# Optimization experiments

Hardware: AMD Instinct MI355X
Metric: run time of the kernel (lower is better)

The kernel has to match this reference:

```python
import jax, jax.numpy as jnp
import numpy as np

IN_BIT = 8      # in_bit_width
W_BIT = 2       # weight_bit_width (also output act quantizer bit width)
BN_EPS = 1e-4


def _ste(x, q):
    # straight-through estimator: forward = q, backward = identity w.r.t. x
    return x + jax.lax.stop_gradient(q - x)


def act_quant(x, bit):
    # CommonActQuant: signed int quant, narrow_range=False, power-of-two scale
    # range [-1, 1 - 2^{-(bit-1)}] -> scale = 2^{-(bit-1)}
    s = 2.0 ** (1 - bit)
    n_min = -(2.0 ** (bit - 1))
    n_max = 2.0 ** (bit - 1) - 1.0
    q = jnp.clip(jnp.round(x / s), n_min, n_max) * s
    return _ste(x, q)


def weight_quant(w, bit):
    # CommonWeightQuant: narrow-range signed int quant, unit scaling const
    # scale = 1 / (2^{bit-1} - 1); for bit=2 levels are {-1, 0, 1}
    n = 2.0 ** (bit - 1) - 1.0
    s = 1.0 / n
    q = jnp.clip(jnp.round(w / s), -n, n) * s
    return _ste(w, q)


def setup_inputs() -> dict:
    key = jax.random.key(0)
    k1, k2, k3, k4 = jax.random.split(key, 4)
    B, C, H, W = 32, 256, 32, 32
    x = jax.random.normal(k1, (B, C, H, W), dtype=jnp.float32) * 0.5
    weight = jax.random.normal(k2, (C, C, 3, 3), dtype=jnp.float32) * 0.5
    gamma = jnp.ones((C,), dtype=jnp.float32)
    beta = jnp.zeros((C,), dtype=jnp.float32)
    running_mean = jax.random.normal(k3, (C,), dtype=jnp.float32) * 0.1
    running_var = jax.random.uniform(k4, (C,), dtype=jnp.float32, minval=0.5, maxval=1.5)
    return {"x": x, "weight": weight, "gamma": gamma, "beta": beta,
            "running_mean": running_mean, "running_var": running_var}


def reference(x, weight, gamma, beta, running_mean, running_var):
    # 1) input QuantIdentity (8-bit, [-1, 1-2^-7], power-of-two scale 2^-7)
    xq = act_quant(x, IN_BIT)
    # 2) QuantConv2d 3x3 stride 1 pad 1, no bias, 2-bit weights
    wq = weight_quant(weight, W_BIT)
    y = jax.lax.conv_general_dilated(
        xq, wq, window_strides=(1, 1), padding=((1, 1), (1, 1)),
        dimension_numbers=("NCHW", "OIHW", "NCHW"))
    # 3) BatchNorm2d (inference, eps=1e-4)
    inv = gamma / jnp.sqrt(running_var + BN_EPS)
    y = y * inv[None, :, None, None] + (beta - running_mean * inv)[None, :, None, None]
    # 4) output QuantIdentity at weight_bit_width bits
    return act_quant(y, W_BIT)
```

## Files before the change

### kernel.cpp

```cpp
#include <hip/hip_runtime.h>
#include <hip/hip_bf16.h>
#include <stdint.h>


typedef int i32x4 __attribute__((ext_vector_type(4)));
typedef float f32x4 __attribute__((ext_vector_type(4)));

__device__ __forceinline__ void gload_lds16(const void* g, const void* lds_byte_ptr) {
    __builtin_amdgcn_global_load_lds(
        (const __attribute__((address_space(1))) unsigned int*)(uintptr_t)g,
        (__attribute__((address_space(3))) unsigned int*)(uintptr_t)lds_byte_ptr,
        16, 0, 0);
}

__global__ __launch_bounds__(256) void quant_w_kernel(const float* __restrict__ w,
                                                      signed char* __restrict__ wq) {
    __shared__ signed char tile[2304];
    const int co = blockIdx.x;
    const int t = threadIdx.x;
#pragma unroll
    for (int p = 0; p < 9; ++p) {
        const int idx = p * 256 + t;
        const float v = w[co * 2304 + idx];
        const int ci = idx / 9;
        const int khkw = idx - 9 * ci;
        const float q = fminf(fmaxf(rintf(v), -1.f), 1.f);
        tile[khkw * 256 + ci] = (signed char)(int)q;
    }
    __syncthreads();
    if (t < 144) {
        *(uint4*)(wq + (size_t)co * 2304 + t * 16) = *(const uint4*)(tile + t * 16);
    }
}

__global__ __launch_bounds__(256) void quant_x_kernel(const float* __restrict__ x,
                                                      signed char* __restrict__ xpad) {
    __shared__ signed char tile[32 * 272];
    const int t = threadIdx.x;
    const int b = blockIdx.x / 34;
    const int hp = blockIdx.x % 34;
    signed char* rowbase = xpad + (size_t)((b * 34 + hp) * 34) * 256;
    const uint4 z = {0u, 0u, 0u, 0u};
    if (hp == 0 || hp == 33) {
        for (int i = t; i < 544; i += 256) *(uint4*)(rowbase + i * 16) = z;
        return;
    }
    const int h = hp - 1;
    const int w = t & 31;
    const int cg = (t >> 5) * 4;
#pragma unroll
    for (int p = 0; p < 8; ++p) {
        const int ci = p * 32 + cg;
        unsigned packed = 0;
#pragma unroll
        for (int k = 0; k < 4; ++k) {
            const float v = x[(((size_t)(b * 256 + ci + k)) * 32 + h) * 32 + w];
            float q = fminf(fmaxf(rintf(__fmul_rn(v, 128.f)), -128.f), 127.f);
            packed |= ((unsigned)(unsigned char)(signed char)(int)q) << (8 * k);
        }
        *(unsigned*)(tile + w * 272 + ci) = packed;
    }
    __syncthreads();
#pragma unroll
    for (int q = 0; q < 2; ++q) {
        const int wp = q * 16 + (t >> 4);
        const int ci16 = (t & 15) * 16;
        uint4 v = *(const uint4*)(tile + wp * 272 + ci16);
        *(uint4*)(rowbase + (size_t)(wp + 1) * 256 + ci16) = v;
    }
    if (t < 32) {
        const int wp = (t >> 4) * 33;
        *(uint4*)(rowbase + (size_t)wp * 256 + (t & 15) * 16) = z;
    }
}

__global__ __launch_bounds__(512) void conv_gemm_kernel(
    const signed char* __restrict__ xpad, const signed char* __restrict__ wq,
    const float* __restrict__ gamma, const float* __restrict__ beta,
    const float* __restrict__ mean, const float* __restrict__ var,
    float* __restrict__ out)
{
    __shared__ signed char As[128 * 64];
    __shared__ signed char Bs[128 * 64];

    const int tid = threadIdx.x;
    const int wv = tid >> 6;
    const int lane = tid & 63;
    const int quad = lane >> 4;
    const int l16 = lane & 15;

    const int m0 = (blockIdx.x >> 1) * 128;
    const int n0 = (blockIdx.x & 1) * 128;
    const int wave_m = wv & 1;
    const int wave_n = wv >> 1;

    i32x4 acc[4][2];
#pragma unroll
    for (int i = 0; i < 4; i++)
#pragma unroll
        for (int j = 0; j < 2; j++) acc[i][j] = (i32x4){0, 0, 0, 0};

    const int srow = tid >> 2;
    const int scic = (tid & 3) * 16;
    const unsigned ldsOff = (unsigned)(wv * 1024);
    const int sb = (m0 + srow) >> 10;
    const int sh = ((m0 + srow) >> 5) & 31;
    const int sw = (m0 + srow) & 31;

    for (int kt = 0; kt < 36; ++kt) {
        const int khkw = kt >> 2;
        const int kh = khkw / 3;
        const int kw = khkw - 3 * kh;
        const int ci0 = (kt & 3) * 64;
        const signed char* ga =
            xpad + (size_t)(((sb * 34 + sh + kh) * 34) + (sw + kw)) * 256 + ci0 + scic;
        gload_lds16(ga, As + ldsOff);
        const signed char* gb = wq + (size_t)(n0 + srow) * 2304 + kt * 64 + scic;
        gload_lds16(gb, Bs + ldsOff);
        __syncthreads();

        i32x4 af[4], bfr[2];
#pragma unroll
        for (int i = 0; i < 4; i++) {
            const int row = wave_m * 64 + i * 16 + l16;
            af[i] = *(const i32x4*)(As + row * 64 + quad * 16);
        }
#pragma unroll
        for (int j = 0; j < 2; j++) {
            const int row = wave_n * 32 + j * 16 + l16;
            bfr[j] = *(const i32x4*)(Bs + row * 64 + quad * 16);
        }
#pragma unroll
        for (int i = 0; i < 4; i++)
#pragma unroll
            for (int j = 0; j < 2; j++)
                acc[i][j] = __builtin_amdgcn_mfma_i32_16x16x64_i8(af[i], bfr[j], acc[i][j], 0, 0, 0);
        __syncthreads();
    }

#pragma unroll
    for (int j = 0; j < 2; j++) {
        const int co = n0 + wave_n * 32 + j * 16 + l16;
        const float iv = __fdiv_rn(gamma[co], __fsqrt_rn(__fadd_rn(var[co], 1e-4f)));
        const float bias = __fsub_rn(beta[co], __fmul_rn(mean[co], iv));
#pragma unroll
        for (int i = 0; i < 4; i++) {
            const int m_base = m0 + wave_m * 64 + i * 16 + quad * 4;
            const int b = m_base >> 10;
            const int h = (m_base >> 5) & 31;
            const int w = m_base & 31;
            f32x4 v;
#pragma unroll
            for (int r = 0; r < 4; r++) {
                const float y = __fmul_rn((float)acc[i][j][r], 0.0078125f);
                const float t = __fadd_rn(__fmul_rn(y, iv), bias);
                float z = rintf(__fmul_rn(t, 2.f));
                z = fminf(fmaxf(z, -2.f), 1.f);
                v[r] = __fmul_rn(z, 0.5f);
            }
            *(f32x4*)(&out[(((size_t)(b * 256 + co)) * 32 + h) * 32 + w]) = v;
        }
    }
}

extern "C" void kernel_launch(void* const* d_in, const int* in_sizes, int n_in,
                              void* d_out, int out_size, void* d_ws, size_t ws_size,
                              hipStream_t stream) {
    const float* x      = (const float*)d_in[0];
    const float* weight = (const float*)d_in[1];
    const float* gamma  = (const float*)d_in[2];
    const float* beta   = (const float*)d_in[3];
    const float* rmean  = (const float*)d_in[4];
    const float* rvar   = (const float*)d_in[5];
    float* out = (float*)d_out;

    signed char* wq   = (signed char*)d_ws;
    signed char* xpad = (signed char*)d_ws + (1 << 20);

    quant_w_kernel<<<256, 256, 0, stream>>>(weight, wq);
    quant_x_kernel<<<1088, 256, 0, stream>>>(x, xpad);
    conv_gemm_kernel<<<512, 512, 0, stream>>>(xpad, wq, gamma, beta, rmean, rvar, out);
}
```

Measured before the change: 123.5 us.

## Stage input halo tile once in LDS and stream pre-swizzled weights from global

The conv GEMM now loads each block's 6x34x256 padded input halo into LDS once, with an XOR swizzle, instead of re-staging an A tile on each of 36 k-steps. This reuses the data across the nine filter taps and removes the per-iteration __syncthreads. The weight quant kernel writes weights in an MFMA-fragment-friendly layout so each wave reads B fragments directly from global memory with double-buffered registers. The trade-off is about 52KB of LDS per block, which can limit occupancy, and more global traffic for the B operand.

```diff
diff --git a/kernel.cpp b/kernel.cpp
--- a/kernel.cpp
+++ b/kernel.cpp
@@ -6,10 +6,10 @@
 typedef int i32x4 __attribute__((ext_vector_type(4)));
 typedef float f32x4 __attribute__((ext_vector_type(4)));
 
-__device__ __forceinline__ void gload_lds16(const void* g, const void* lds_byte_ptr) {
+__device__ __forceinline__ void gload_lds16(const void* g, const void* lds) {
     __builtin_amdgcn_global_load_lds(
         (const __attribute__((address_space(1))) unsigned int*)(uintptr_t)g,
-        (__attribute__((address_space(3))) unsigned int*)(uintptr_t)lds_byte_ptr,
+        (__attribute__((address_space(3))) unsigned int*)(uintptr_t)lds,
         16, 0, 0);
 }
 
@@ -29,7 +29,9 @@
     }
     __syncthreads();
     if (t < 144) {
-        *(uint4*)(wq + (size_t)co * 2304 + t * 16) = *(const uint4*)(tile + t * 16);
+        const int kt = t >> 2, kq = t & 3;
+        const uint4 v = *(const uint4*)(tile + t * 16);
+        *(uint4*)(wq + ((size_t)((co >> 4) * 36 + kt) << 10) + kq * 256 + (co & 15) * 16) = v;
     }
 }
 
@@ -74,25 +76,43 @@
     }
 }
 
-__global__ __launch_bounds__(512) void conv_gemm_kernel(
-    const signed char* __restrict__ xpad, const signed char* __restrict__ wq,
+__global__ __launch_bounds__(512, 4) void conv_gemm_kernel(
+    const signed char* __restrict__ xpad, const signed char* __restrict__ wqm,
     const float* __restrict__ gamma, const float* __restrict__ beta,
     const float* __restrict__ mean, const float* __restrict__ var,
     float* __restrict__ out)
 {
-    __shared__ signed char As[128 * 64];
-    __shared__ signed char Bs[128 * 64];
+    __shared__ signed char As[6 * 34 * 256];
 
     const int tid = threadIdx.x;
     const int wv = tid >> 6;
     const int lane = tid & 63;
-    const int quad = lane >> 4;
     const int l16 = lane & 15;
+    const int l4 = lane >> 4;
 
-    const int m0 = (blockIdx.x >> 1) * 128;
+    const int mt = blockIdx.x >> 1;
     const int n0 = (blockIdx.x & 1) * 128;
+    const int b = mt >> 3;
+    const int h0 = (mt & 7) * 4;
     const int wave_m = wv & 1;
     const int wave_n = wv >> 1;
+
+    const signed char* xbase = xpad + (size_t)(b * 34 + h0) * 34 * 256;
+    for (int i = wv; i < 51; i += 8) {
+        const int d = i * 64 + lane;
+        const int r = d >> 4;
+        const int c = d & 15;
+        gload_lds16(xbase + r * 256 + ((c ^ (r & 15)) << 4), As + i * 1024);
+    }
+    __syncthreads();
+
+    int r0[4];
+#pragma unroll
+    for (int i = 0; i < 4; ++i)
+        r0[i] = (wave_m * 2 + (i >> 1)) * 34 + (i & 1) * 16 + l16;
+
+    const signed char* bp0 = wqm + (((size_t)((n0 >> 4) + wave_n * 2 + 0) * 36) << 10) + lane * 16;
+    const signed char* bp1 = wqm + (((size_t)((n0 >> 4) + wave_n * 2 + 1) * 36) << 10) + lane * 16;
 
     i32x4 acc[4][2];
 #pragma unroll
@@ -100,55 +120,45 @@
 #pragma unroll
         for (int j = 0; j < 2; j++) acc[i][j] = (i32x4){0, 0, 0, 0};
 
-    const int srow = tid >> 2;
-    const int scic = (tid & 3) * 16;
-    const unsigned ldsOff = (unsigned)(wv * 1024);
-    const int sb = (m0 + srow) >> 10;
-    const int sh = ((m0 + srow) >> 5) & 31;
-    const int sw = (m0 + srow) & 31;
+    i32x4 aA[4], bA[2], aB[4], bB[2];
 
-    for (int kt = 0; kt < 36; ++kt) {
-        const int khkw = kt >> 2;
-        const int kh = khkw / 3;
-        const int kw = khkw - 3 * kh;
-        const int ci0 = (kt & 3) * 64;
-        const signed char* ga =
-            xpad + (size_t)(((sb * 34 + sh + kh) * 34) + (sw + kw)) * 256 + ci0 + scic;
-        gload_lds16(ga, As + ldsOff);
-        const signed char* gb = wq + (size_t)(n0 + srow) * 2304 + kt * 64 + scic;
-        gload_lds16(gb, Bs + ldsOff);
-        __syncthreads();
+#define LOAD_B(kt, dst) { dst[0] = *(const i32x4*)(bp0 + (kt) * 1024); \
+                          dst[1] = *(const i32x4*)(bp1 + (kt) * 1024); }
+#define LOAD_A(kt, dst) { const int khkw = (kt) >> 2; \
+                          const int kh = khkw / 3; \
+                          const int kw = khkw - 3 * kh; \
+                          const int roff = kh * 34 + kw; \
+                          const int cb = ((kt) & 3) * 4 + l4; \
+                          _Pragma("unroll") \
+                          for (int i = 0; i < 4; ++i) { \
+                              const int r = r0[i] + roff; \
+                              dst[i] = *(const i32x4*)(As + r * 256 + ((cb ^ (r & 15)) << 4)); \
+                          } }
+#define MFMA(af, bf) { _Pragma("unroll") \
+                       for (int i = 0; i < 4; ++i) \
+                           _Pragma("unroll") \
+                           for (int j = 0; j < 2; ++j) \
+                               acc[i][j] = __builtin_amdgcn_mfma_i32_16x16x64_i8(af[i], bf[j], acc[i][j], 0, 0, 0); }
 
-        i32x4 af[4], bfr[2];
-#pragma unroll
-        for (int i = 0; i < 4; i++) {
-            const int row = wave_m * 64 + i * 16 + l16;
-            af[i] = *(const i32x4*)(As + row * 64 + quad * 16);
-        }
-#pragma unroll
-        for (int j = 0; j < 2; j++) {
-            const int row = wave_n * 32 + j * 16 + l16;
-            bfr[j] = *(const i32x4*)(Bs + row * 64 + quad * 16);
-        }
-#pragma unroll
-        for (int i = 0; i < 4; i++)
-#pragma unroll
-            for (int j = 0; j < 2; j++)
-                acc[i][j] = __builtin_amdgcn_mfma_i32_16x16x64_i8(af[i], bfr[j], acc[i][j], 0, 0, 0);
-        __syncthreads();
+    LOAD_B(0, bA)
+    LOAD_A(0, aA)
+    for (int kt = 0; kt < 36; kt += 2) {
+        LOAD_B(kt + 1, bB)
+        LOAD_A(kt + 1, aB)
+        MFMA(aA, bA)
+        if (kt + 2 < 36) { LOAD_B(kt + 2, bA) LOAD_A(kt + 2, aA) }
+        MFMA(aB, bB)
     }
 
 #pragma unroll
-    for (int j = 0; j < 2; j++) {
+    for (int j = 0; j < 2; ++j) {
         const int co = n0 + wave_n * 32 + j * 16 + l16;
         const float iv = __fdiv_rn(gamma[co], __fsqrt_rn(__fadd_rn(var[co], 1e-4f)));
         const float bias = __fsub_rn(beta[co], __fmul_rn(mean[co], iv));
 #pragma unroll
-        for (int i = 0; i < 4; i++) {
-            const int m_base = m0 + wave_m * 64 + i * 16 + quad * 4;
-            const int b = m_base >> 10;
-            const int h = (m_base >> 5) & 31;
-            const int w = m_base & 31;
+        for (int i = 0; i < 4; ++i) {
+            const int h = h0 + wave_m * 2 + (i >> 1);
+            const int w = (i & 1) * 16 + l4 * 4;
             f32x4 v;
 #pragma unroll
             for (int r = 0; r < 4; r++) {
@@ -161,6 +171,9 @@
             *(f32x4*)(&out[(((size_t)(b * 256 + co)) * 32 + h) * 32 + w]) = v;
         }
     }
+#undef LOAD_B
+#undef LOAD_A
+#undef MFMA
 }
 
 extern "C" void kernel_launch(void* const* d_in, const int* in_sizes, int n_in,
```

After: 118.2 us. 4.3% less time.
